# Kernel optimization log

Measured on AMD Instinct MI355X. Metric: run time of the kernel, lower is better.

The kernel has to match this reference:

```python
import jax, jax.numpy as jnp
import numpy as np

CUTOFF = 5.0
BOX = 20.0
EPS = 1e-5


def _neighbor_list_np(cutoff, coords, cell):
    # coords: [N,3] float32, cell: [3,3]. Returns (pair_first, pair_second, pair_image)
    inv_cell = np.linalg.inv(cell)
    proj = coords @ inv_cell
    frac = np.fmod(proj, 1.0)                      # matches torch.fmod (sign-preserving)
    woff = np.floor(proj).astype(np.int64)          # torch.div(..., rounding_mode='floor')
    wrapped = (frac @ cell).astype(coords.dtype)
    inv_lengths = np.linalg.norm(inv_cell, axis=0)
    nb = (np.floor(cutoff * inv_lengths + EPS) + 1).astype(np.int64)
    ranges = [np.arange(-int(n), int(n) + 1) for n in nb]
    # image grid ordered (i1 outer, i2, i3 inner) to match the nested torch loops
    images = np.stack(np.meshgrid(*ranges, indexing='ij'), axis=-1).reshape(-1, 3)
    off_cart = images.astype(coords.dtype) @ cell   # [K,3]
    drij = wrapped[:, None, :] - wrapped[None, :, :]           # [N,N,3]
    diff = drij[None, :, :, :] + off_cart[:, None, None, :]    # [K,N,N,3]
    dist = np.linalg.norm(diff, axis=-1)                       # [K,N,N]
    mask = dist < cutoff
    zero_k = int(np.where((images == 0).all(axis=1))[0][0])
    np.fill_diagonal(mask[zero_k], False)                      # drop self pairs in home image
    k, i, j = np.nonzero(mask)  # row-major (k,i,j) == per-image blocks of (i,j), same order as torch
    woff_ij = woff[i] - woff[j]
    pair_image = images[k] - woff_ij
    return i, j, pair_image


def setup_inputs() -> dict:
    key = jax.random.key(0)
    n_mol, n_at = 16, 512
    coordinates = jax.random.uniform(key, (n_mol, n_at, 3), dtype=jnp.float32) * BOX
    nonblank = jnp.ones((n_mol, n_at), dtype=bool)
    real_atoms = jnp.arange(n_mol * n_at, dtype=jnp.int32)
    inv_real_atoms = jnp.arange(n_mol * n_at, dtype=jnp.int32)
    cell = jnp.tile((BOX * jnp.eye(3, dtype=jnp.float32))[None], (n_mol, 1, 1))
    mol_index = jnp.arange(n_mol * n_at, dtype=jnp.int32) // n_at
    return dict(coordinates=coordinates, nonblank=nonblank, real_atoms=real_atoms,
                inv_real_atoms=inv_real_atoms, cell=cell, mol_index=mol_index,
                n_molecules=n_mol, n_atoms_max=n_at)


def reference(coordinates, nonblank, real_atoms, inv_real_atoms, cell, mol_index,
              n_molecules, n_atoms_max):
    # --- neighbor-list construction (torch.no_grad section): host numpy, vectorized over images ---
    coords_np = np.asarray(coordinates)
    cell_np = np.asarray(cell)
    nb_np = np.asarray(nonblank)
    pfs, pss, ofs = [], [], []
    for m in range(n_molecules):
        r = coords_np[m][nb_np[m]]
        pf, ps, of = _neighbor_list_np(CUTOFF, r, cell_np[m])
        if len(pf) == 0:
            continue
        pfs.append(pf + m * n_atoms_max)
        pss.append(ps + m * n_atoms_max)
        ofs.append(of)
    pf = np.concatenate(pfs)
    ps = np.concatenate(pss)
    of = np.concatenate(ofs)
    n_images = max(1, int(np.abs(of).max()))

    pair_first = inv_real_atoms[jnp.asarray(pf)]
    pair_second = inv_real_atoms[jnp.asarray(ps)]
    offsets = jnp.asarray(of.astype(np.int32))
    n_off = 2 * n_images + 1
    o1, o2, o3 = (offsets + n_images).T
    offset_index = o3 + n_off * (o2 + n_off * o1)
    pair_mol = mol_index[pair_first]
    pair_cell = cell[pair_mol]                                   # [P,3,3]
    pair_offsets = jnp.einsum('pk,pkl->pl', offsets.astype(cell.dtype), pair_cell)

    # --- differentiable distance evaluation ---
    coordflat = coordinates.reshape(n_molecules * n_atoms_max, 3)[real_atoms]
    paircoord = coordflat[pair_first] - coordflat[pair_second] + pair_offsets
    distflat2 = jnp.linalg.norm(paircoord, axis=1)
    return distflat2, pair_first, pair_second, paircoord, offsets, offset_index
```

## Files before the change

### kernel.cpp

```cpp
#include <hip/hip_runtime.h>

#define NMOL 16
#define NAT  512
#define NK   27
#define NCHUNK (NMOL * NK)

#define SSMAX 24.999998092651367f

__device__ __forceinline__ float wrap1(float v) {
    return __fmul_rn(__fmul_rn(v, 0.05f), 20.0f);
}

__device__ __forceinline__ int probe_code(float wx, float wy, float wz,
                                          float wjx, float wjy, float wjz,
                                          bool self) {
    float dx = __fsub_rn(wx, wjx);
    float dy = __fsub_rn(wy, wjy);
    float dz = __fsub_rn(wz, wjz);
    int ox = (dx > 15.0f) ? -1 : ((dx < -15.0f) ? 1 : 0);
    int oy = (dy > 15.0f) ? -1 : ((dy < -15.0f) ? 1 : 0);
    int oz = (dz > 15.0f) ? -1 : ((dz < -15.0f) ? 1 : 0);
    float ax = __fadd_rn(dx, 20.0f * (float)ox);
    float ay = __fadd_rn(dy, 20.0f * (float)oy);
    float az = __fadd_rn(dz, 20.0f * (float)oz);
    float ss = __fadd_rn(__fadd_rn(__fmul_rn(ax, ax), __fmul_rn(ay, ay)),
                         __fmul_rn(az, az));
    bool hit = (ss < SSMAX) && !self;
    return hit ? ((ox + 1) * 9 + (oy + 1) * 3 + (oz + 1)) : 31;
}

__global__ __launch_bounds__(256, 8) void pass_count(const float* __restrict__ coords,
                                                     int* __restrict__ cnt) {
    __shared__ float rr[NAT * 3];
    __shared__ int cur[2][4][NK];
    const int blk  = blockIdx.x;
    const int m    = blk >> 6;
    const int g0   = (blk & 63) * 2;
    const int t    = threadIdx.x;
    const int w    = t >> 6;
    const int lane = t & 63;
    const int iA   = g0 * 4 + w;
    const int iB   = iA + 4;

    const float4* cm4 = reinterpret_cast<const float4*>(coords + (size_t)m * NAT * 3);
    float4* rr4 = reinterpret_cast<float4*>(rr);
    rr4[t] = cm4[t];
    if (t < 128) rr4[t + 256] = cm4[t + 256];
    if (t < 2 * 4 * NK) ((int*)cur)[t] = 0;
    __syncthreads();

    const float wAx = wrap1(rr[iA * 3 + 0]), wAy = wrap1(rr[iA * 3 + 1]), wAz = wrap1(rr[iA * 3 + 2]);
    const float wBx = wrap1(rr[iB * 3 + 0]), wBy = wrap1(rr[iB * 3 + 1]), wBz = wrap1(rr[iB * 3 + 2]);

    #pragma unroll
    for (int it = 0; it < NAT / 64; ++it) {
        const int j = it * 64 + lane;
        float wjx = wrap1(rr[j * 3 + 0]);
        float wjy = wrap1(rr[j * 3 + 1]);
        float wjz = wrap1(rr[j * 3 + 2]);
        int cA = probe_code(wAx, wAy, wAz, wjx, wjy, wjz, j == iA);
        int cB = probe_code(wBx, wBy, wBz, wjx, wjy, wjz, j == iB);
        if (cA != 31) atomicAdd(&cur[0][w][cA], 1);
        if (cB != 31) atomicAdd(&cur[1][w][cB], 1);
    }
    __syncthreads();
    if (t < 216) {
        int uu = t / 108, rem = t % 108, ww = rem / 27, k = rem % 27;
        int i = (g0 + uu) * 4 + ww;
        cnt[(m * NK + k) * NAT + i] = cur[uu][ww][k];
    }
}

__global__ __launch_bounds__(512) void scan_chunk(int* __restrict__ cnt,
                                                  int* __restrict__ sums) {
    __shared__ int wsum[8], wexc[9];
    const int c = blockIdx.x;
    const int t = threadIdx.x;
    const int w = t >> 6;
    const int lane = t & 63;
    const int idx = c * 512 + t;
    const int orig = cnt[idx];
    int v = orig;
    #pragma unroll
    for (int d = 1; d < 64; d <<= 1) {
        int u = __shfl_up(v, d, 64);
        if (lane >= d) v += u;
    }
    if (lane == 63) wsum[w] = v;
    __syncthreads();
    if (t < 8) {
        int s = 0;
        for (int q = 0; q < t; ++q) s += wsum[q];
        wexc[t] = s;
        if (t == 7) wexc[8] = s + wsum[7];
    }
    __syncthreads();
    cnt[idx] = wexc[w] + (v - orig);
    if (t == 0) sums[c] = wexc[8];
}

__global__ __launch_bounds__(256, 8) void pass_emit(const float* __restrict__ coords,
                                                    const int* __restrict__ cnt,
                                                    const int* __restrict__ sums,
                                                    float* __restrict__ out, int P) {
    __shared__ float rr[NAT * 3];
    __shared__ int sbuf[NCHUNK];
    __shared__ int wsum4[4], wexc4[4];
    __shared__ int cur[2][4][NK];
    const int blk  = blockIdx.x;
    const int m    = blk >> 6;
    const int g0   = (blk & 63) * 2;
    const int t    = threadIdx.x;
    const int w    = t >> 6;
    const int lane = t & 63;

    const float4* cm4 = reinterpret_cast<const float4*>(coords + (size_t)m * NAT * 3);
    float4* rr4 = reinterpret_cast<float4*>(rr);
    rr4[t] = cm4[t];
    if (t < 128) rr4[t + 256] = cm4[t + 256];

    const int e0 = 2 * t;
    int v0 = (e0 < NCHUNK) ? sums[e0] : 0;
    int v1 = (e0 + 1 < NCHUNK) ? sums[e0 + 1] : 0;
    const int ps = v0 + v1;
    int incl = ps;
    #pragma unroll
    for (int d = 1; d < 64; d <<= 1) {
        int u = __shfl_up(incl, d, 64);
        if (lane >= d) incl += u;
    }
    if (lane == 63) wsum4[w] = incl;
    __syncthreads();
    if (t < 4) {
        int s = 0;
        for (int q = 0; q < t; ++q) s += wsum4[q];
        wexc4[t] = s;
    }
    __syncthreads();
    const int pe = wexc4[w] + (incl - ps);
    if (e0 < NCHUNK)     sbuf[e0]     = pe;
    if (e0 + 1 < NCHUNK) sbuf[e0 + 1] = pe + v0;
    __syncthreads();
    if (t < 216) {
        int uu = t / 108, rem = t % 108, ww = rem / 27, k = rem % 27;
        int c  = m * NK + k;
        int i  = (g0 + uu) * 4 + ww;
        cur[uu][ww][k] = cnt[c * NAT + i] + sbuf[c];
    }
    __syncthreads();

    const int iA = g0 * 4 + w, iB = iA + 4;
    const float rAx = rr[iA * 3 + 0], rAy = rr[iA * 3 + 1], rAz = rr[iA * 3 + 2];
    const float rBx = rr[iB * 3 + 0], rBy = rr[iB * 3 + 1], rBz = rr[iB * 3 + 2];
    const float wAx = wrap1(rAx), wAy = wrap1(rAy), wAz = wrap1(rAz);
    const float wBx = wrap1(rBx), wBy = wrap1(rBy), wBz = wrap1(rBz);
    const unsigned long long ltmask =
        (lane == 0) ? 0ull : (~0ull >> (64 - lane));

    #pragma unroll
    for (int it = 0; it < NAT / 64; ++it) {
        const int j = it * 64 + lane;
        const float rjx = rr[j * 3 + 0], rjy = rr[j * 3 + 1], rjz = rr[j * 3 + 2];
        const float wjx = wrap1(rjx), wjy = wrap1(rjy), wjz = wrap1(rjz);

        #pragma unroll
        for (int uu = 0; uu < 2; ++uu) {
            const int i  = (uu == 0) ? iA : iB;
            const float rx = (uu == 0) ? rAx : rBx;
            const float ry = (uu == 0) ? rAy : rBy;
            const float rz = (uu == 0) ? rAz : rBz;
            int code = (uu == 0)
                ? probe_code(wAx, wAy, wAz, wjx, wjy, wjz, j == iA)
                : probe_code(wBx, wBy, wBz, wjx, wjy, wjz, j == iB);
            bool hit = (code != 31);
            int kk = hit ? code : 0;

            unsigned long long grp = __ballot(hit);
            #pragma unroll
            for (int b = 0; b < 5; ++b) {
                unsigned long long bm = __ballot((kk >> b) & 1);
                grp &= ((kk >> b) & 1) ? bm : ~bm;
            }
            int leader = hit ? (__ffsll((unsigned long long)grp) - 1) : 0;
            int cntg   = __popcll(grp);
            int rank   = __popcll(grp & ltmask);

            int base = 0;
            if (hit && lane == leader)
                base = atomicAdd(&cur[uu][w][kk], cntg);
            base = __shfl(base, leader, 64);

            if (hit) {
                int p = base + rank;
                if (p < P) {
                    int ox = kk / 9;
                    int rem = kk - ox * 9;
                    int oy = rem / 3;
                    int oz = rem - oy * 3;
                    ox -= 1; oy -= 1; oz -= 1;
                    float cx = 20.0f * (float)ox;
                    float cy = 20.0f * (float)oy;
                    float cz = 20.0f * (float)oz;
                    float px = __fadd_rn(__fsub_rn(rx, rjx), cx);
                    float py = __fadd_rn(__fsub_rn(ry, rjy), cy);
                    float pz = __fadd_rn(__fsub_rn(rz, rjz), cz);
                    float ss = __fadd_rn(__fadd_rn(__fmul_rn(px, px), __fmul_rn(py, py)),
                                         __fmul_rn(pz, pz));
                    out[p]                 = __fsqrt_rn(ss);
                    out[P + p]             = (float)(m * NAT + i);
                    out[2 * P + p]         = (float)(m * NAT + j);
                    out[3 * P + 3 * p + 0] = px;
                    out[3 * P + 3 * p + 1] = py;
                    out[3 * P + 3 * p + 2] = pz;
                    out[6 * P + 3 * p + 0] = (float)ox;
                    out[6 * P + 3 * p + 1] = (float)oy;
                    out[6 * P + 3 * p + 2] = (float)oz;
                    out[9 * P + p]         = (float)kk;
                }
            }
        }
    }
}

extern "C" void kernel_launch(void* const* d_in, const int* in_sizes, int n_in,
                              void* d_out, int out_size, void* d_ws, size_t ws_size,
                              hipStream_t stream) {
    (void)in_sizes; (void)n_in; (void)ws_size;
    const float* coords = (const float*)d_in[0];
    int* cnt  = (int*)d_ws;
    int* sums = cnt + NMOL * NK * NAT;
    float* out = (float*)d_out;
    const int P = out_size / 10;

    hipLaunchKernelGGL(pass_count, dim3(NMOL * NAT / 8), dim3(256), 0, stream, coords, cnt);
    hipLaunchKernelGGL(scan_chunk, dim3(NCHUNK), dim3(512), 0, stream, cnt, sums);
    hipLaunchKernelGGL(pass_emit, dim3(NMOL * NAT / 8), dim3(256), 0, stream,
                       coords, cnt, sums, out, P);
}
```

Before: 97.71 us.

## Fuse count, scan and emit into one kernel with a grid barrier

Replaces the three launches (count, per-chunk scan, emit) with one 64-block kernel. Each block handles a quarter of one molecule's rows but recomputes that molecule's full 27x512 count table and scan in LDS. Blocks then sync through a global atomic spin barrier to exchange per-molecule totals before emitting. This removes launch gaps and global round-trips for the count table, but leaves only 64 blocks on a large GPU, does the count work four times over, and depends on every block being co-resident for the spin barrier.

```diff
diff --git a/kernel.cpp b/kernel.cpp
--- a/kernel.cpp
+++ b/kernel.cpp
@@ -3,7 +3,7 @@
 #define NMOL 16
 #define NAT  512
 #define NK   27
-#define NCHUNK (NMOL * NK)
+#define NBLK 64
 
 #define SSMAX 24.999998092651367f
 
@@ -29,149 +29,104 @@
     return hit ? ((ox + 1) * 9 + (oy + 1) * 3 + (oz + 1)) : 31;
 }
 
-__global__ __launch_bounds__(256, 8) void pass_count(const float* __restrict__ coords,
-                                                     int* __restrict__ cnt) {
+__global__ __launch_bounds__(1024, 4) void fused(const float* __restrict__ coords,
+                                                 int* __restrict__ bar,
+                                                 int* __restrict__ totals,
+                                                 float* __restrict__ out, int P) {
     __shared__ float rr[NAT * 3];
-    __shared__ int cur[2][4][NK];
+    __shared__ int cnt[NK * NAT];
+    __shared__ int ctot[NK];
+    __shared__ int cexcl[NK];
+    __shared__ int tls[NMOL];
+
     const int blk  = blockIdx.x;
-    const int m    = blk >> 6;
-    const int g0   = (blk & 63) * 2;
-    const int t    = threadIdx.x;
-    const int w    = t >> 6;
-    const int lane = t & 63;
-    const int iA   = g0 * 4 + w;
-    const int iB   = iA + 4;
-
-    const float4* cm4 = reinterpret_cast<const float4*>(coords + (size_t)m * NAT * 3);
-    float4* rr4 = reinterpret_cast<float4*>(rr);
-    rr4[t] = cm4[t];
-    if (t < 128) rr4[t + 256] = cm4[t + 256];
-    if (t < 2 * 4 * NK) ((int*)cur)[t] = 0;
-    __syncthreads();
-
-    const float wAx = wrap1(rr[iA * 3 + 0]), wAy = wrap1(rr[iA * 3 + 1]), wAz = wrap1(rr[iA * 3 + 2]);
-    const float wBx = wrap1(rr[iB * 3 + 0]), wBy = wrap1(rr[iB * 3 + 1]), wBz = wrap1(rr[iB * 3 + 2]);
-
-    #pragma unroll
-    for (int it = 0; it < NAT / 64; ++it) {
-        const int j = it * 64 + lane;
-        float wjx = wrap1(rr[j * 3 + 0]);
-        float wjy = wrap1(rr[j * 3 + 1]);
-        float wjz = wrap1(rr[j * 3 + 2]);
-        int cA = probe_code(wAx, wAy, wAz, wjx, wjy, wjz, j == iA);
-        int cB = probe_code(wBx, wBy, wBz, wjx, wjy, wjz, j == iB);
-        if (cA != 31) atomicAdd(&cur[0][w][cA], 1);
-        if (cB != 31) atomicAdd(&cur[1][w][cB], 1);
-    }
-    __syncthreads();
-    if (t < 216) {
-        int uu = t / 108, rem = t % 108, ww = rem / 27, k = rem % 27;
-        int i = (g0 + uu) * 4 + ww;
-        cnt[(m * NK + k) * NAT + i] = cur[uu][ww][k];
-    }
-}
-
-__global__ __launch_bounds__(512) void scan_chunk(int* __restrict__ cnt,
-                                                  int* __restrict__ sums) {
-    __shared__ int wsum[8], wexc[9];
-    const int c = blockIdx.x;
-    const int t = threadIdx.x;
-    const int w = t >> 6;
-    const int lane = t & 63;
-    const int idx = c * 512 + t;
-    const int orig = cnt[idx];
-    int v = orig;
-    #pragma unroll
-    for (int d = 1; d < 64; d <<= 1) {
-        int u = __shfl_up(v, d, 64);
-        if (lane >= d) v += u;
-    }
-    if (lane == 63) wsum[w] = v;
-    __syncthreads();
-    if (t < 8) {
-        int s = 0;
-        for (int q = 0; q < t; ++q) s += wsum[q];
-        wexc[t] = s;
-        if (t == 7) wexc[8] = s + wsum[7];
-    }
-    __syncthreads();
-    cnt[idx] = wexc[w] + (v - orig);
-    if (t == 0) sums[c] = wexc[8];
-}
-
-__global__ __launch_bounds__(256, 8) void pass_emit(const float* __restrict__ coords,
-                                                    const int* __restrict__ cnt,
-                                                    const int* __restrict__ sums,
-                                                    float* __restrict__ out, int P) {
-    __shared__ float rr[NAT * 3];
-    __shared__ int sbuf[NCHUNK];
-    __shared__ int wsum4[4], wexc4[4];
-    __shared__ int cur[2][4][NK];
-    const int blk  = blockIdx.x;
-    const int m    = blk >> 6;
-    const int g0   = (blk & 63) * 2;
+    const int m    = blk >> 2;
+    const int q    = blk & 3;
     const int t    = threadIdx.x;
     const int w    = t >> 6;
     const int lane = t & 63;
 
     const float4* cm4 = reinterpret_cast<const float4*>(coords + (size_t)m * NAT * 3);
     float4* rr4 = reinterpret_cast<float4*>(rr);
-    rr4[t] = cm4[t];
-    if (t < 128) rr4[t + 256] = cm4[t + 256];
+    if (t < 384) rr4[t] = cm4[t];
+    for (int x = t; x < NK * NAT; x += 1024) cnt[x] = 0;
+    __syncthreads();
 
-    const int e0 = 2 * t;
-    int v0 = (e0 < NCHUNK) ? sums[e0] : 0;
-    int v1 = (e0 + 1 < NCHUNK) ? sums[e0 + 1] : 0;
-    const int ps = v0 + v1;
-    int incl = ps;
-    #pragma unroll
-    for (int d = 1; d < 64; d <<= 1) {
-        int u = __shfl_up(incl, d, 64);
-        if (lane >= d) incl += u;
-    }
-    if (lane == 63) wsum4[w] = incl;
-    __syncthreads();
-    if (t < 4) {
-        int s = 0;
-        for (int q = 0; q < t; ++q) s += wsum4[q];
-        wexc4[t] = s;
-    }
-    __syncthreads();
-    const int pe = wexc4[w] + (incl - ps);
-    if (e0 < NCHUNK)     sbuf[e0]     = pe;
-    if (e0 + 1 < NCHUNK) sbuf[e0 + 1] = pe + v0;
-    __syncthreads();
-    if (t < 216) {
-        int uu = t / 108, rem = t % 108, ww = rem / 27, k = rem % 27;
-        int c  = m * NK + k;
-        int i  = (g0 + uu) * 4 + ww;
-        cur[uu][ww][k] = cnt[c * NAT + i] + sbuf[c];
+    for (int u = 0; u < 16; ++u) {
+        const int iA = w * 32 + 2 * u, iB = iA + 1;
+        const float wAx = wrap1(rr[iA*3+0]), wAy = wrap1(rr[iA*3+1]), wAz = wrap1(rr[iA*3+2]);
+        const float wBx = wrap1(rr[iB*3+0]), wBy = wrap1(rr[iB*3+1]), wBz = wrap1(rr[iB*3+2]);
+        #pragma unroll
+        for (int it = 0; it < NAT / 64; ++it) {
+            const int j = it * 64 + lane;
+            const float wjx = wrap1(rr[j*3+0]);
+            const float wjy = wrap1(rr[j*3+1]);
+            const float wjz = wrap1(rr[j*3+2]);
+            int cA = probe_code(wAx, wAy, wAz, wjx, wjy, wjz, j == iA);
+            int cB = probe_code(wBx, wBy, wBz, wjx, wjy, wjz, j == iB);
+            if (cA != 31) atomicAdd(&cnt[cA * NAT + iA], 1);
+            if (cB != 31) atomicAdd(&cnt[cB * NAT + iB], 1);
+        }
     }
     __syncthreads();
 
-    const int iA = g0 * 4 + w, iB = iA + 4;
-    const float rAx = rr[iA * 3 + 0], rAy = rr[iA * 3 + 1], rAz = rr[iA * 3 + 2];
-    const float rBx = rr[iB * 3 + 0], rBy = rr[iB * 3 + 1], rBz = rr[iB * 3 + 2];
-    const float wAx = wrap1(rAx), wAy = wrap1(rAy), wAz = wrap1(rAz);
-    const float wBx = wrap1(rBx), wBy = wrap1(rBy), wBz = wrap1(rBz);
+    for (int k = w; k < NK; k += 16) {
+        int* ck = cnt + k * NAT;
+        int v[8];
+        int tot = 0;
+        #pragma unroll
+        for (int e = 0; e < 8; ++e) { v[e] = ck[lane * 8 + e]; tot += v[e]; }
+        int incl = tot;
+        #pragma unroll
+        for (int d = 1; d < 64; d <<= 1) {
+            int uu = __shfl_up(incl, d, 64);
+            if (lane >= d) incl += uu;
+        }
+        int acc = incl - tot;
+        #pragma unroll
+        for (int e = 0; e < 8; ++e) { int tmp = v[e]; ck[lane * 8 + e] = acc; acc += tmp; }
+        if (lane == 63) ctot[k] = incl;
+    }
+    __syncthreads();
+
+    if (t == 0) {
+        if (q == 0) {
+            int mt = 0;
+            for (int k = 0; k < NK; ++k) mt += ctot[k];
+            __hip_atomic_store(&totals[m], mt, __ATOMIC_RELAXED, __HIP_MEMORY_SCOPE_AGENT);
+        }
+        __hip_atomic_fetch_add(bar, 1, __ATOMIC_ACQ_REL, __HIP_MEMORY_SCOPE_AGENT);
+        while (__hip_atomic_load(bar, __ATOMIC_ACQUIRE, __HIP_MEMORY_SCOPE_AGENT) < NBLK)
+            __builtin_amdgcn_s_sleep(2);
+    }
+    __syncthreads();
+    if (t < NMOL)
+        tls[t] = __hip_atomic_load(&totals[t], __ATOMIC_RELAXED, __HIP_MEMORY_SCOPE_AGENT);
+    __syncthreads();
+    if (t == 0) {
+        int run = 0;
+        for (int mm = 0; mm < m; ++mm) run += tls[mm];
+        for (int k = 0; k < NK; ++k) { cexcl[k] = run; run += ctot[k]; }
+    }
+    __syncthreads();
+    for (int x = t; x < NK * NAT; x += 1024) cnt[x] += cexcl[x >> 9];
+    __syncthreads();
+
     const unsigned long long ltmask =
         (lane == 0) ? 0ull : (~0ull >> (64 - lane));
 
-    #pragma unroll
-    for (int it = 0; it < NAT / 64; ++it) {
-        const int j = it * 64 + lane;
-        const float rjx = rr[j * 3 + 0], rjy = rr[j * 3 + 1], rjz = rr[j * 3 + 2];
-        const float wjx = wrap1(rjx), wjy = wrap1(rjy), wjz = wrap1(rjz);
+    for (int u = 0; u < 8; ++u) {
+        const int i  = q * 128 + w * 8 + u;
+        const float rx = rr[i*3+0], ry = rr[i*3+1], rz = rr[i*3+2];
+        const float wx = wrap1(rx), wy = wrap1(ry), wz = wrap1(rz);
+        const int pf = m * NAT + i;
 
         #pragma unroll
-        for (int uu = 0; uu < 2; ++uu) {
-            const int i  = (uu == 0) ? iA : iB;
-            const float rx = (uu == 0) ? rAx : rBx;
-            const float ry = (uu == 0) ? rAy : rBy;
-            const float rz = (uu == 0) ? rAz : rBz;
-            int code = (uu == 0)
-                ? probe_code(wAx, wAy, wAz, wjx, wjy, wjz, j == iA)
-                : probe_code(wBx, wBy, wBz, wjx, wjy, wjz, j == iB);
+        for (int it = 0; it < NAT / 64; ++it) {
+            const int j = it * 64 + lane;
+            const float rjx = rr[j*3+0], rjy = rr[j*3+1], rjz = rr[j*3+2];
+            int code = probe_code(wx, wy, wz,
+                                  wrap1(rjx), wrap1(rjy), wrap1(rjz), j == i);
             bool hit = (code != 31);
             int kk = hit ? code : 0;
 
@@ -187,7 +142,7 @@
 
             int base = 0;
             if (hit && lane == leader)
-                base = atomicAdd(&cur[uu][w][kk], cntg);
+                base = atomicAdd(&cnt[kk * NAT + i], cntg);
             base = __shfl(base, leader, 64);
 
             if (hit) {
@@ -207,7 +162,7 @@
                     float ss = __fadd_rn(__fadd_rn(__fmul_rn(px, px), __fmul_rn(py, py)),
                                          __fmul_rn(pz, pz));
                     out[p]                 = __fsqrt_rn(ss);
-                    out[P + p]             = (float)(m * NAT + i);
+                    out[P + p]             = (float)pf;
                     out[2 * P + p]         = (float)(m * NAT + j);
                     out[3 * P + 3 * p + 0] = px;
                     out[3 * P + 3 * p + 1] = py;
@@ -227,13 +182,12 @@
                               hipStream_t stream) {
     (void)in_sizes; (void)n_in; (void)ws_size;
     const float* coords = (const float*)d_in[0];
-    int* cnt  = (int*)d_ws;
-    int* sums = cnt + NMOL * NK * NAT;
-    float* out = (float*)d_out;
-    const int P = out_size / 10;
+    int* bar    = (int*)d_ws;
+    int* totals = bar + 16;
+    float* out  = (float*)d_out;
+    int P = out_size / 10;
 
-    hipLaunchKernelGGL(pass_count, dim3(NMOL * NAT / 8), dim3(256), 0, stream, coords, cnt);
-    hipLaunchKernelGGL(scan_chunk, dim3(NCHUNK), dim3(512), 0, stream, cnt, sums);
-    hipLaunchKernelGGL(pass_emit, dim3(NMOL * NAT / 8), dim3(256), 0, stream,
-                       coords, cnt, sums, out, P);
+    hipMemsetAsync(bar, 0, 64, stream);
+    hipLaunchKernelGGL(fused, dim3(NBLK), dim3(1024), 0, stream,
+                       coords, bar, totals, out, P);
 }
```

New measurement: 193.4 us. +97.9%, slower.
